# Optimization experiments

Hardware: AMD Instinct MI355X
Metric: run time of the kernel (lower is better)

The kernel has to match this reference:

```python
import jax, jax.numpy as jnp
import numpy as np

U, B, S, R = 64, 256, 256, 512
N = 4096
EMA_DECAY = 0.99


def setup_inputs() -> dict:
    key = jax.random.key(0)
    ks = jax.random.split(key, 9)
    q_u = jax.random.uniform(ks[0], (N, U), dtype=jnp.float32)
    q_b = jax.random.uniform(ks[1], (N, B), dtype=jnp.float32)
    q_sigma = jax.random.normal(ks[2], (N, S), dtype=jnp.float32)
    delta_rule_target = jax.random.normal(ks[3], (N, R), dtype=jnp.float32)
    write_mask = jax.random.randint(ks[4], (N,), 0, 2).astype(bool)
    delta_rule_proto = 0.02 * jax.random.normal(ks[5], (U, B, R), dtype=jnp.float32)
    signature_proto = 0.02 * jax.random.normal(ks[6], (U, B, S), dtype=jnp.float32)
    ema_conf = jax.random.uniform(ks[7], (U, B), dtype=jnp.float32)
    usage_count = jnp.maximum(jax.random.uniform(ks[8], (U, B)) - 0.5, 0.0) * 100.0
    return {"q_u": q_u, "q_b": q_b, "q_sigma": q_sigma,
            "delta_rule_target": delta_rule_target, "write_mask": write_mask,
            "delta_rule_proto": delta_rule_proto, "signature_proto": signature_proto,
            "ema_conf": ema_conf, "usage_count": usage_count}


def _l2norm(x):
    return x / jnp.maximum(jnp.linalg.norm(x, axis=-1, keepdims=True), 1e-12)


def reference(q_u, q_b, q_sigma, delta_rule_target, write_mask,
              delta_rule_proto, signature_proto, ema_conf, usage_count):
    # ---------------- retrieve ----------------
    # joint attention over (operator, binding) cells; temperature == 1.0 branch
    joint = q_u[:, :, None] * q_b[:, None, :]                  # [N, U, B]
    valid = (usage_count > 0).astype(joint.dtype)              # [U, B]
    w = joint * valid
    denom = w.sum(axis=(-2, -1), keepdims=True)
    w = jnp.where(denom > 0, w / jnp.maximum(denom, 1e-6), jnp.zeros_like(w))
    memory_delta_rule = jnp.einsum('nub,ubr->nr', w, delta_rule_proto)
    memory_signature = jnp.einsum('nub,ubs->ns', w, signature_proto)
    base_conf = jnp.einsum('nub,ub->n', w, ema_conf)[:, None]  # [N, 1]
    cos = jnp.sum(_l2norm(q_sigma) * _l2norm(memory_signature + 1e-6),
                  axis=-1, keepdims=True)
    signature_agreement = 0.5 * (1.0 + cos)
    memory_conf = jnp.clip(base_conf * signature_agreement, 0.0, 1.0)

    # ---------------- update (vectorized scatter EMA) ----------------
    m = write_mask.astype(q_u.dtype)                           # [N]
    op_conf = q_u.max(axis=-1)
    op_id = jnp.argmax(q_u, axis=-1)
    bind_conf = q_b.max(axis=-1)
    bind_id = jnp.argmax(q_b, axis=-1)
    write_conf = op_conf * bind_conf                           # [N]
    cell = op_id * B + bind_id                                 # [N]
    num_cells = U * B
    wgt = write_conf * m
    sum_w = jax.ops.segment_sum(wgt, cell, num_segments=num_cells)          # [UB]
    sum_d = jax.ops.segment_sum(delta_rule_target * wgt[:, None], cell,
                                num_segments=num_cells)                     # [UB, R]
    sum_s = jax.ops.segment_sum(q_sigma * wgt[:, None], cell,
                                num_segments=num_cells)                     # [UB, S]
    cnt = jax.ops.segment_sum(m, cell, num_segments=num_cells)              # [UB]
    conf_sum = jnp.maximum(sum_w, 1e-6)
    delta_mean = (sum_d / conf_sum[:, None]).reshape(U, B, R)
    sigma_mean = (sum_s / conf_sum[:, None]).reshape(U, B, S)
    conf_mean = (sum_w / jnp.maximum(cnt, 1.0)).reshape(U, B)
    upd = (cnt > 0).reshape(U, B)
    new_delta_proto = jnp.where(upd[:, :, None],
                                EMA_DECAY * delta_rule_proto + (1.0 - EMA_DECAY) * delta_mean,
                                delta_rule_proto)
    new_signature_proto = jnp.where(upd[:, :, None],
                                    EMA_DECAY * signature_proto + (1.0 - EMA_DECAY) * sigma_mean,
                                    signature_proto)
    new_ema_conf = jnp.where(upd,
                             EMA_DECAY * ema_conf + (1.0 - EMA_DECAY) * conf_mean,
                             ema_conf)
    new_usage = usage_count + cnt.reshape(U, B)

    # ---------------- usage stats ----------------
    write_rate = m.mean()
    usage_fraction = (new_usage > 0).astype(jnp.float32).mean()
    dist = new_usage.reshape(-1)
    dist = dist / jnp.maximum(dist.sum(), 1e-6)
    usage_entropy = -(dist * jnp.log(dist + 1e-6)).sum() / np.log(max(2, num_cells))

    return (memory_delta_rule, memory_signature, memory_conf,
            new_delta_proto, new_signature_proto, new_ema_conf, new_usage,
            write_rate, usage_fraction, usage_entropy)
```

## Files before the change

### kernel.cpp

```cpp
#include <hip/hip_runtime.h>
#include <hip/hip_fp8.h>
#include <math.h>

#define NR 4096
#define UD 64
#define BD 256
#define SD 256
#define RD 512
#define UBD 16384
#define DECAY 0.99f

typedef unsigned char u8;
typedef __attribute__((ext_vector_type(4))) float f32x4;
typedef __attribute__((ext_vector_type(2))) long longx2;

#define OFF_MDR   0ull
#define OFF_MSIG  2097152ull
#define OFF_MCONF 3145728ull
#define OFF_NDP   3149824ull
#define OFF_NSP   11538432ull
#define OFF_NEC   15732736ull
#define OFF_NUS   15749120ull
#define OFF_SCAL  15765504ull

static __device__ __forceinline__ u8 f2e4m3(float x) {
  __hip_fp8_e4m3 h(x);
  return (u8)h.__x;
}

static __device__ __forceinline__ void gll16(const void* g, void* l) {
  __builtin_amdgcn_global_load_lds(
      (const __attribute__((address_space(1))) unsigned int*)g,
      (__attribute__((address_space(3))) unsigned int*)l, 16, 0, 0);
}

static __device__ __forceinline__ int perm64(int x) {
  return (((x >> 3) & 3) << 4) | (((x >> 5) & 1) << 3) | (x & 7);
}

__global__ __launch_bounds__(256) void row_prep_kernel(
    const float* __restrict__ q_u, const float* __restrict__ q_b,
    const float* __restrict__ usage, const float* __restrict__ ema,
    const unsigned char* __restrict__ wm,
    float* __restrict__ denom, float* __restrict__ base_raw,
    float* __restrict__ wgt, int* __restrict__ cellid, float* __restrict__ mrow,
    float* __restrict__ sum_w, float* __restrict__ cnt)
{
  const int r0 = blockIdx.x * 16;
  const int t = threadIdx.x;
  __shared__ float s_qu[16][64];
  __shared__ float s_qbv[16][256];
  __shared__ float s_pd[16][256];
  __shared__ float s_pc[16][256];
  __shared__ int s_flag;
  {
    const float4 v = *(const float4*)(q_u + (size_t)r0 * UD + t * 4);
    float* dst = &s_qu[0][0] + t * 4;
    dst[0] = v.x; dst[1] = v.y; dst[2] = v.z; dst[3] = v.w;
  }
  {
    const float4* src = (const float4*)(q_b + (size_t)r0 * BD);
    float4* dst = (float4*)&s_qbv[0][0];
    #pragma unroll
    for (int i = 0; i < 4; ++i) dst[t + i * 256] = src[t + i * 256];
  }
  if (t == 0) {
    const int*   wi = (const int*)wm;
    const float* wf = (const float*)wm;
    bool is_i32 = true, is_f32 = true;
    #pragma unroll
    for (int i = 0; i < 16; ++i) {
      int v = wi[i];
      if (v != 0 && v != 1) is_i32 = false;
      float f = wf[i];
      if (f != 0.f && f != 1.f) is_f32 = false;
    }
    s_flag = is_i32 ? 2 : (is_f32 ? 1 : 0);
  }
  __syncthreads();
  float accd[16], accc[16];
  #pragma unroll
  for (int r = 0; r < 16; ++r) { accd[r] = 0.f; accc[r] = 0.f; }
  #pragma unroll 2
  for (int u = 0; u < UD; ++u) {
    const float us = usage[u * BD + t];
    const float em = ema[u * BD + t];
    const float vm = (us > 0.f) ? 1.f : 0.f;
    const float ev = em * vm;
    #pragma unroll
    for (int r = 0; r < 16; ++r) {
      accd[r] += s_qu[r][u] * vm;
      accc[r] += s_qu[r][u] * ev;
    }
  }
  #pragma unroll
  for (int r = 0; r < 16; ++r) {
    s_pd[r][t] = accd[r] * s_qbv[r][t];
    s_pc[r][t] = accc[r] * s_qbv[r][t];
  }
  __syncthreads();
  const int w = t >> 6, l = t & 63;
  #pragma unroll
  for (int rr = 0; rr < 4; ++rr) {
    const int row = w * 4 + rr;
    float dsum = s_pd[row][l] + s_pd[row][l + 64] + s_pd[row][l + 128] + s_pd[row][l + 192];
    float csum = s_pc[row][l] + s_pc[row][l + 64] + s_pc[row][l + 128] + s_pc[row][l + 192];
    #pragma unroll
    for (int m = 1; m < 64; m <<= 1) {
      dsum += __shfl_xor(dsum, m);
      csum += __shfl_xor(csum, m);
    }
    float bv_ = s_qbv[row][l]; int bi_ = l;
    #pragma unroll
    for (int k = 1; k < 4; ++k) {
      const float v2 = s_qbv[row][l + k * 64];
      if (v2 > bv_) { bv_ = v2; bi_ = l + k * 64; }
    }
    #pragma unroll
    for (int m = 1; m < 64; m <<= 1) {
      const float ov = __shfl_xor(bv_, m);
      const int   oi = __shfl_xor(bi_, m);
      if (ov > bv_ || (ov == bv_ && oi < bi_)) { bv_ = ov; bi_ = oi; }
    }
    float uv_ = s_qu[row][l]; int ui_ = l;
    #pragma unroll
    for (int m = 1; m < 64; m <<= 1) {
      const float ov = __shfl_xor(uv_, m);
      const int   oi = __shfl_xor(ui_, m);
      if (ov > uv_ || (ov == uv_ && oi < ui_)) { uv_ = ov; ui_ = oi; }
    }
    if (l == 0) {
      const int n = r0 + row;
      const int fm = s_flag;
      float m;
      if (fm == 2)      m = (((const int*)wm)[n]   != 0)   ? 1.f : 0.f;
      else if (fm == 1) m = (((const float*)wm)[n] != 0.f) ? 1.f : 0.f;
      else              m = (wm[n] != 0)   ? 1.f : 0.f;
      const float wv = uv_ * bv_ * m;
      const int cell = ui_ * BD + bi_;
      denom[n]    = dsum;
      base_raw[n] = csum;
      wgt[n]      = wv;
      cellid[n]   = cell;
      mrow[n]     = m;
      if (m != 0.f) {
        atomicAdd(&sum_w[cell], wv);
        atomicAdd(&cnt[cell], 1.f);
      }
    }
  }
}

__global__ __launch_bounds__(256) void prep_kernel(
    const float* __restrict__ qb, const float* __restrict__ qu,
    u8* __restrict__ qb8, float* __restrict__ quT)
{
  if (blockIdx.x < 1024) {
    const int i = blockIdx.x * 256 + threadIdx.x;
    const int idx = i * 4;
    const int row = idx >> 8;
    const int b   = idx & 255;
    const float4 v = *(const float4*)(qb + (size_t)idx);
    u8 tmp[4] = { f2e4m3(v.x), f2e4m3(v.y), f2e4m3(v.z), f2e4m3(v.w) };
    unsigned int wv; __builtin_memcpy(&wv, tmp, 4);
    const int nb = (b & ~63) | perm64(b & 63);
    *(unsigned int*)(qb8 + (size_t)row * BD + nb) = wv;
  } else {
    __shared__ float s[64][65];
    const int n0 = (blockIdx.x - 1024) * 64;
    const int tid = threadIdx.x;
    #pragma unroll
    for (int i = 0; i < 16; ++i) {
      const int idx = tid + i * 256;
      const int r = idx >> 6, u = idx & 63;
      s[r][u] = qu[(size_t)(n0 + r) * UD + u];
    }
    __syncthreads();
    #pragma unroll
    for (int i = 0; i < 16; ++i) {
      const int idx = tid + i * 256;
      const int u = idx >> 6, r = idx & 63;
      quT[(size_t)u * NR + n0 + r] = s[r][u];
    }
  }
}

__global__ __launch_bounds__(256) void transpose_mask_kernel(
    const float* __restrict__ dproto, const float* __restrict__ sproto,
    const float* __restrict__ usage, u8* __restrict__ PT8)
{
  __shared__ u8 s[64][68];
  const int k0 = blockIdx.x * 64;
  const int rblk = blockIdx.y;
  const float* src; int ld; int c0s;
  if (rblk < 8) { src = dproto; ld = RD; c0s = rblk * 64; }
  else          { src = sproto; ld = SD; c0s = (rblk - 8) * 64; }
  const int tid = threadIdx.x;
  const int kl = tid >> 4;
  const int rl = (tid & 15) * 4;
  #pragma unroll
  for (int i = 0; i < 4; ++i) {
    const int k = kl + i * 16;
    const bool valid = usage[k0 + k] > 0.f;
    const float4 v = *(const float4*)(src + (size_t)(k0 + k) * ld + c0s + rl);
    s[k][rl + 0] = valid ? f2e4m3(v.x) : (u8)0;
    s[k][rl + 1] = valid ? f2e4m3(v.y) : (u8)0;
    s[k][rl + 2] = valid ? f2e4m3(v.z) : (u8)0;
    s[k][rl + 3] = valid ? f2e4m3(v.w) : (u8)0;
  }
  __syncthreads();
  const int rl2 = tid >> 4;
  const int kl2 = (tid & 15) * 4;
  #pragma unroll
  for (int i = 0; i < 4; ++i) {
    const int r = rl2 + i * 16;
    u8 tmp[4] = { s[kl2 + 0][r], s[kl2 + 1][r], s[kl2 + 2][r], s[kl2 + 3][r] };
    unsigned int wv; __builtin_memcpy(&wv, tmp, 4);
    *(unsigned int*)(PT8 + (size_t)(rblk * 64 + r) * UBD + k0 + perm64(kl2)) = wv;
  }
}

__global__ __launch_bounds__(256, 3) void mfma_gemm_kernel(
    const float* __restrict__ quT, const u8* __restrict__ qb8,
    const u8* __restrict__ PT8, float* __restrict__ out,
    int* __restrict__ tk, int* __restrict__ gf, int* __restrict__ claimed)
{
  __shared__ u8 sA[2][128 * 128];
  __shared__ u8 sB[2][128 * 64];
  __shared__ int s_work;
  const int tid = threadIdx.x;

  if (tid == 0) {
    unsigned int xcc;
    asm volatile("s_getreg_b32 %0, hwreg(HW_REG_XCC_ID)" : "=s"(xcc));
    const int x = (int)(xcc & 7u);
    const int t = atomicAdd(&tk[x], 1);
    int w = -1;
    if (t < 96) {
      const int cand = x * 96 + t;
      if (atomicCAS(&claimed[cand], 0, 1) == 0) w = cand;
    }
    while (w < 0) {
      const int g = atomicAdd(gf, 1);
      if (g >= 768) { w = -2; break; }
      if (atomicCAS(&claimed[g], 0, 1) == 0) w = g;
    }
    s_work = w;
  }
  __syncthreads();
  const int w = s_work;
  if (w < 0) return;

  const int bx = w & 31;
  const int combo = w >> 5;
  const int by = combo >> 2;
  const int bz = combo & 3;

  const int wid = tid >> 6, lane = tid & 63;
  const int n0 = bx * 128;
  const int kbeg = bz * (UBD / 4);

  float* obase; int ldO; int cc0;
  if (by < 4) { obase = out + OFF_MDR;  ldO = RD; cc0 = by * 128; }
  else        { obase = out + OFF_MSIG; ldO = SD; cc0 = (by - 4) * 128; }
  const int c0 = by * 128;

  const int lrowA = lane >> 3;
  const int csrcA = ((lane & 7) ^ lrowA) * 16;
  const u8* gA = qb8 + (size_t)(n0 + lrowA) * BD + csrcA;
  const int lrowB = lane >> 2;
  const int srcslotB = (lane & 3) ^ ((lrowB >> 1) & 3);
  const u8* gB = PT8 + (size_t)(c0 + wid * 16 + lrowB) * UBD + kbeg + srcslotB * 16;

  const int wr = (wid >> 1) * 64, wc = (wid & 1) * 64;
  const int fr = lane & 15;
  const int kg = lane >> 4;
  int aoff[4], boff[4];
  #pragma unroll
  for (int m = 0; m < 4; ++m) aoff[m] = (wr + m * 16 + fr) * 128;
  #pragma unroll
  for (int nn = 0; nn < 4; ++nn) boff[nn] = (wc + nn * 16 + fr) * 64;
  int slothA[2];
  #pragma unroll
  for (int bq = 0; bq < 2; ++bq) slothA[bq] = ((bq * 4 + kg) ^ (fr & 7)) * 16;
  const int slotB16 = (kg ^ ((fr >> 1) & 3)) * 16;

  f32x4 accm[4][4];
  #pragma unroll
  for (int m = 0; m < 4; ++m)
    #pragma unroll
    for (int nn = 0; nn < 4; ++nn)
      accm[m][nn] = (f32x4){0.f, 0.f, 0.f, 0.f};

  #pragma unroll
  for (int i = 0; i < 4; ++i) {
    const int ro = wid * 32 + i * 8;
    gll16(gA + (size_t)ro * BD,       &sA[0][ro * 128]);
    gll16(gA + (size_t)ro * BD + 128, &sA[1][ro * 128]);
  }
  #pragma unroll
  for (int i = 0; i < 2; ++i)
    gll16(gB + (size_t)(i * 64) * UBD, &sB[0][(i * 64 + wid * 16) * 64]);
  __syncthreads();

  const float* quTb = quT + n0 + wr + kg * 4;
  const int ubase = kbeg >> 8;
  f32x4 accu[4][4];

  for (int ph = 0; ph < 64; ++ph) {
    const int buf  = ph & 1;
    const int half = (ph >> 1) & 1;
    const int bq   = ph & 1;
    if (ph < 63) {
      const u8* gs = gB + (size_t)(ph + 1) * 64;
      #pragma unroll
      for (int i = 0; i < 2; ++i)
        gll16(gs + (size_t)(i * 64) * UBD, &sB[buf ^ 1][(i * 64 + wid * 16) * 64]);
    }
    const u8* sa = sA[half];
    const u8* sb = sB[buf];
    longx2 av[4], bv[4];
    #pragma unroll
    for (int m = 0; m < 4; ++m)
      av[m] = *(const longx2*)(sa + aoff[m] + slothA[bq]);
    #pragma unroll
    for (int nn = 0; nn < 4; ++nn)
      bv[nn] = *(const longx2*)(sb + boff[nn] + slotB16);
    const bool first = (ph & 3) == 0;
    #pragma unroll
    for (int m = 0; m < 4; ++m)
      #pragma unroll
      for (int nn = 0; nn < 4; ++nn) {
        if (first)
          accu[m][nn] = __builtin_amdgcn_mfma_f32_16x16x32_fp8_fp8(
              av[m].x, bv[nn].x, (f32x4){0.f, 0.f, 0.f, 0.f}, 0, 0, 0);
        else
          accu[m][nn] = __builtin_amdgcn_mfma_f32_16x16x32_fp8_fp8(
              av[m].x, bv[nn].x, accu[m][nn], 0, 0, 0);
        accu[m][nn] = __builtin_amdgcn_mfma_f32_16x16x32_fp8_fp8(
            av[m].y, bv[nn].y, accu[m][nn], 0, 0, 0);
      }
    __syncthreads();
    if ((ph & 3) == 3) {
      const float* qp = quTb + (size_t)(ubase + (ph >> 2)) * NR;
      #pragma unroll
      for (int m = 0; m < 4; ++m) {
        const f32x4 qv = *(const f32x4*)(qp + m * 16);
        #pragma unroll
        for (int nn = 0; nn < 4; ++nn)
          accm[m][nn] += qv * accu[m][nn];
      }
    }
  }

  #pragma unroll
  for (int m = 0; m < 4; ++m) {
    #pragma unroll
    for (int nn = 0; nn < 4; ++nn) {
      const int c = cc0 + wc + nn * 16 + fr;
      #pragma unroll
      for (int j = 0; j < 4; ++j) {
        const int r = n0 + wr + m * 16 + kg * 4 + j;
        atomicAdd(obase + (size_t)r * ldO + c, accm[m][nn][j]);
      }
    }
  }
}

__global__ __launch_bounds__(256) void epilogue_kernel(
    const float* __restrict__ q_sigma, const float* __restrict__ denom,
    const float* __restrict__ base_raw, float* __restrict__ out)
{
  const int n = blockIdx.x;
  const int t = threadIdx.x;
  __shared__ float r1[256], r2[256], r3[256];
  const float d = denom[n];
  const float scale = (d > 0.f) ? (1.f / fmaxf(d, 1e-6f)) : 0.f;
  float* mdr = out + OFF_MDR + (size_t)n * RD;
  mdr[t]       *= scale;
  mdr[t + 256] *= scale;
  float* msig = out + OFF_MSIG + (size_t)n * SD;
  const float s = msig[t] * scale;
  msig[t] = s;
  const float a = q_sigma[(size_t)n * SD + t];
  const float b = s + 1e-6f;
  r1[t] = a * a; r2[t] = b * b; r3[t] = a * b;
  __syncthreads();
  for (int st = 128; st > 0; st >>= 1) {
    if (t < st) { r1[t] += r1[t + st]; r2[t] += r2[t + st]; r3[t] += r3[t + st]; }
    __syncthreads();
  }
  if (t == 0) {
    const float na = fmaxf(sqrtf(r1[0]), 1e-12f);
    const float nb = fmaxf(sqrtf(r2[0]), 1e-12f);
    const float cosv = r3[0] / (na * nb);
    const float agree = 0.5f * (1.f + cosv);
    const float base = (d > 0.f) ? base_raw[n] / fmaxf(d, 1e-6f) : 0.f;
    out[OFF_MCONF + n] = fminf(fmaxf(base * agree, 0.f), 1.f);
  }
}

__global__ __launch_bounds__(256) void ema_copy_kernel(
    const float* __restrict__ dproto, const float* __restrict__ sproto,
    const float* __restrict__ cnt,
    float* __restrict__ outd, float* __restrict__ outs)
{
  const size_t nd = (size_t)UBD * RD;
  const size_t total = nd + (size_t)UBD * SD;
  for (size_t i = (size_t)blockIdx.x * 256 + threadIdx.x; i < total;
       i += (size_t)gridDim.x * 256) {
    if (i < nd) {
      const float p = dproto[i];
      outd[i] = (cnt[(int)(i >> 9)] > 0.f) ? DECAY * p : p;
    } else {
      const size_t j = i - nd;
      const float p = sproto[j];
      outs[j] = (cnt[(int)(j >> 8)] > 0.f) ? DECAY * p : p;
    }
  }
}

__global__ __launch_bounds__(256) void scatter2_kernel(
    const float* __restrict__ dtarget, const float* __restrict__ q_sigma,
    const float* __restrict__ wgt, const int* __restrict__ cellid,
    const float* __restrict__ mrow, const float* __restrict__ sum_w,
    float* __restrict__ outd, float* __restrict__ outs)
{
  const int n = blockIdx.x;
  if (mrow[n] == 0.f) return;
  const int t = threadIdx.x;
  const int c = cellid[n];
  const float cs = fmaxf(sum_w[c], 1e-6f);
  const float coef = (1.0f - DECAY) * wgt[n] / cs;
  atomicAdd(&outd[(size_t)c * RD + t],       dtarget[(size_t)n * RD + t] * coef);
  atomicAdd(&outd[(size_t)c * RD + t + 256], dtarget[(size_t)n * RD + t + 256] * coef);
  atomicAdd(&outs[(size_t)c * SD + t],       q_sigma[(size_t)n * SD + t] * coef);
}

__global__ __launch_bounds__(256) void ema_small_kernel(
    const float* __restrict__ ema, const float* __restrict__ usage,
    const float* __restrict__ sum_w, const float* __restrict__ cnt,
    float* __restrict__ out_ec, float* __restrict__ out_us)
{
  const int i = blockIdx.x * 256 + threadIdx.x;
  if (i < UBD) {
    const float c = cnt[i];
    const float cm = sum_w[i] / fmaxf(c, 1.f);
    out_ec[i] = (c > 0.f) ? DECAY * ema[i] + (1.f - DECAY) * cm : ema[i];
    out_us[i] = usage[i] + c;
  }
}

__global__ __launch_bounds__(256) void stats_kernel(
    const float* __restrict__ cnt, const float* __restrict__ new_us,
    float* __restrict__ out_scalars)
{
  const int t = threadIdx.x;
  __shared__ float r1[256], r2[256], r3[256];
  float scnt = 0.f, snz = 0.f, sus = 0.f;
  for (int i = t; i < UBD; i += 256) {
    const float c = cnt[i]; scnt += c;
    const float u = new_us[i];
    if (u > 0.f) snz += 1.f;
    sus += u;
  }
  r1[t] = scnt; r2[t] = snz; r3[t] = sus;
  __syncthreads();
  for (int s = 128; s > 0; s >>= 1) {
    if (t < s) { r1[t] += r1[t + s]; r2[t] += r2[t + s]; r3[t] += r3[t + s]; }
    __syncthreads();
  }
  const float total_cnt = r1[0], total_nz = r2[0], total_us = r3[0];
  __syncthreads();
  const float S = fmaxf(total_us, 1e-6f);
  float ent = 0.f;
  for (int i = t; i < UBD; i += 256) {
    const float d = new_us[i] / S;
    ent += d * logf(d + 1e-6f);
  }
  r1[t] = ent;
  __syncthreads();
  for (int s = 128; s > 0; s >>= 1) {
    if (t < s) { r1[t] += r1[t + s]; }
    __syncthreads();
  }
  if (t == 0) {
    out_scalars[0] = total_cnt / (float)NR;
    out_scalars[1] = total_nz / (float)UBD;
    out_scalars[2] = -r1[0] / 9.70406053f;
  }
}

extern "C" void kernel_launch(void* const* d_in, const int* in_sizes, int n_in,
                              void* d_out, int out_size, void* d_ws, size_t ws_size,
                              hipStream_t stream)
{
  const float* q_u    = (const float*)d_in[0];
  const float* q_b    = (const float*)d_in[1];
  const float* q_sig  = (const float*)d_in[2];
  const float* dtg    = (const float*)d_in[3];
  const unsigned char* wm = (const unsigned char*)d_in[4];
  const float* dproto = (const float*)d_in[5];
  const float* sproto = (const float*)d_in[6];
  const float* ema    = (const float*)d_in[7];
  const float* usage  = (const float*)d_in[8];
  float* out = (float*)d_out;

  float* wsf = (float*)d_ws;
  int*   wsi = (int*)d_ws;
  float* denom    = wsf + 16;
  float* base_raw = wsf + 16 + 4096;
  float* wgtb     = wsf + 16 + 8192;
  int*   cellid   = wsi + 16 + 12288;
  float* mrow     = wsf + 16 + 16384;
  float* sum_w    = wsf + 20496;
  float* cnt      = wsf + 20496 + 16384;
  int*   tk       = wsi + 53264;
  int*   gf       = wsi + 53272;
  int*   claimed  = wsi + 53280;

  u8*    PT8 = (u8*)(out + OFF_NDP);
  u8*    qb8 = PT8 + (size_t)768 * UBD;
  float* quT = (float*)(qb8 + (size_t)NR * BD);

  prep_kernel<<<1024 + NR / 64, 256, 0, stream>>>(q_b, q_u, qb8, quT);
  transpose_mask_kernel<<<dim3(UBD / 64, 12), 256, 0, stream>>>(dproto, sproto,
                                                                usage, PT8);
  hipMemsetAsync(out, 0, (size_t)OFF_MCONF * sizeof(float), stream);
  hipMemsetAsync(sum_w, 0, (2u * UBD + 16 + 768) * sizeof(float), stream);

  row_prep_kernel<<<NR / 16, 256, 0, stream>>>(q_u, q_b, usage, ema, wm,
                                               denom, base_raw, wgtb, cellid, mrow,
                                               sum_w, cnt);
  mfma_gemm_kernel<<<768, 256, 0, stream>>>(quT, qb8, PT8, out, tk, gf, claimed);
  epilogue_kernel<<<NR, 256, 0, stream>>>(q_sig, denom, base_raw, out);

  ema_copy_kernel<<<4096, 256, 0, stream>>>(dproto, sproto, cnt,
                                            out + OFF_NDP, out + OFF_NSP);
  scatter2_kernel<<<NR, 256, 0, stream>>>(dtg, q_sig, wgtb, cellid, mrow, sum_w,
                                          out + OFF_NDP, out + OFF_NSP);
  ema_small_kernel<<<UBD / 256, 256, 0, stream>>>(ema, usage, sum_w, cnt,
                                                  out + OFF_NEC, out + OFF_NUS);
  stats_kernel<<<1, 256, 0, stream>>>(cnt, out + OFF_NUS, out + OFF_SCAL);
}
```

Baseline: 221.7 us.

## Remove split-K from FP8 retrieval GEMM and keep A fragments in registers

The retrieval GEMM drops its 4-way split-K with atomicAdd outputs. It now uses 256 workgroups, each covering 128 rows by 96 columns over the full K range. The q_b FP8 fragments stay in registers, q_u is staged once in LDS, and the prototype tiles stream through a 6-stage LDS ring driven by explicit vmcnt waits. The denominator scaling moves into the GEMM store, which removes the output memset and the read-modify-write in the epilogue. The cost is fewer workgroups (one per CU at launch_bounds 1), longer serial K loops and higher register pressure.

After: 352.6 us. 59.1% more time.

```diff
diff --git a/kernel.cpp b/kernel.cpp
--- a/kernel.cpp
+++ b/kernel.cpp
@@ -220,15 +220,17 @@
   }
 }
 
-__global__ __launch_bounds__(256, 3) void mfma_gemm_kernel(
+__global__ __launch_bounds__(256, 1) void mfma_gemm_kernel(
     const float* __restrict__ quT, const u8* __restrict__ qb8,
-    const u8* __restrict__ PT8, float* __restrict__ out,
+    const u8* __restrict__ PT8, const float* __restrict__ denom,
+    float* __restrict__ out,
     int* __restrict__ tk, int* __restrict__ gf, int* __restrict__ claimed)
 {
-  __shared__ u8 sA[2][128 * 128];
-  __shared__ u8 sB[2][128 * 64];
+  __shared__ __attribute__((aligned(16))) u8 smB[6 * 96 * 128];
+  __shared__ __attribute__((aligned(16))) float squT[64 * 128];
   __shared__ int s_work;
   const int tid = threadIdx.x;
+  const int wid = tid >> 6, lane = tid & 63;
 
   if (tid == 0) {
     unsigned int xcc;
@@ -236,13 +238,13 @@
     const int x = (int)(xcc & 7u);
     const int t = atomicAdd(&tk[x], 1);
     int w = -1;
-    if (t < 96) {
-      const int cand = x * 96 + t;
+    if (t < 32) {
+      const int cand = x * 32 + t;
       if (atomicCAS(&claimed[cand], 0, 1) == 0) w = cand;
     }
     while (w < 0) {
       const int g = atomicAdd(gf, 1);
-      if (g >= 768) { w = -2; break; }
+      if (g >= 256) { w = -2; break; }
       if (atomicCAS(&claimed[g], 0, 1) == 0) w = g;
     }
     s_work = w;
@@ -251,139 +253,135 @@
   const int w = s_work;
   if (w < 0) return;
 
+  const int ct = w >> 5;
   const int bx = w & 31;
-  const int combo = w >> 5;
-  const int by = combo >> 2;
-  const int bz = combo & 3;
-
-  const int wid = tid >> 6, lane = tid & 63;
   const int n0 = bx * 128;
-  const int kbeg = bz * (UBD / 4);
-
-  float* obase; int ldO; int cc0;
-  if (by < 4) { obase = out + OFF_MDR;  ldO = RD; cc0 = by * 128; }
-  else        { obase = out + OFF_MSIG; ldO = SD; cc0 = (by - 4) * 128; }
-  const int c0 = by * 128;
-
-  const int lrowA = lane >> 3;
-  const int csrcA = ((lane & 7) ^ lrowA) * 16;
-  const u8* gA = qb8 + (size_t)(n0 + lrowA) * BD + csrcA;
-  const int lrowB = lane >> 2;
-  const int srcslotB = (lane & 3) ^ ((lrowB >> 1) & 3);
-  const u8* gB = PT8 + (size_t)(c0 + wid * 16 + lrowB) * UBD + kbeg + srcslotB * 16;
-
-  const int wr = (wid >> 1) * 64, wc = (wid & 1) * 64;
+  const int c0 = ct * 96;
+
   const int fr = lane & 15;
   const int kg = lane >> 4;
-  int aoff[4], boff[4];
-  #pragma unroll
-  for (int m = 0; m < 4; ++m) aoff[m] = (wr + m * 16 + fr) * 128;
-  #pragma unroll
-  for (int nn = 0; nn < 4; ++nn) boff[nn] = (wc + nn * 16 + fr) * 64;
-  int slothA[2];
-  #pragma unroll
-  for (int bq = 0; bq < 2; ++bq) slothA[bq] = ((bq * 4 + kg) ^ (fr & 7)) * 16;
-  const int slotB16 = (kg ^ ((fr >> 1) & 3)) * 16;
-
-  f32x4 accm[4][4];
-  #pragma unroll
-  for (int m = 0; m < 4; ++m)
-    #pragma unroll
-    for (int nn = 0; nn < 4; ++nn)
-      accm[m][nn] = (f32x4){0.f, 0.f, 0.f, 0.f};
-
-  #pragma unroll
-  for (int i = 0; i < 4; ++i) {
-    const int ro = wid * 32 + i * 8;
-    gll16(gA + (size_t)ro * BD,       &sA[0][ro * 128]);
-    gll16(gA + (size_t)ro * BD + 128, &sA[1][ro * 128]);
-  }
-  #pragma unroll
-  for (int i = 0; i < 2; ++i)
-    gll16(gB + (size_t)(i * 64) * UBD, &sB[0][(i * 64 + wid * 16) * 64]);
-  __syncthreads();
-
-  const float* quTb = quT + n0 + wr + kg * 4;
-  const int ubase = kbeg >> 8;
-  f32x4 accu[4][4];
-
-  for (int ph = 0; ph < 64; ++ph) {
-    const int buf  = ph & 1;
-    const int half = (ph >> 1) & 1;
-    const int bq   = ph & 1;
-    if (ph < 63) {
-      const u8* gs = gB + (size_t)(ph + 1) * 64;
-      #pragma unroll
-      for (int i = 0; i < 2; ++i)
-        gll16(gs + (size_t)(i * 64) * UBD, &sB[buf ^ 1][(i * 64 + wid * 16) * 64]);
-    }
-    const u8* sa = sA[half];
-    const u8* sb = sB[buf];
-    longx2 av[4], bv[4];
-    #pragma unroll
-    for (int m = 0; m < 4; ++m)
-      av[m] = *(const longx2*)(sa + aoff[m] + slothA[bq]);
-    #pragma unroll
-    for (int nn = 0; nn < 4; ++nn)
-      bv[nn] = *(const longx2*)(sb + boff[nn] + slotB16);
-    const bool first = (ph & 3) == 0;
+  const int wr = (wid >> 1) * 64;
+  const int wcol = (wid & 1) * 48;
+
+  const int lrow = lane >> 3;
+  const int ssl  = ((lane & 7) ^ lrow) * 16;
+  const u8* gB = PT8 + (size_t)(c0 + wid * 24 + lrow) * UBD + ssl;
+
+  int boff[3];
+  #pragma unroll
+  for (int nn = 0; nn < 3; ++nn)
+    boff[nn] = (wcol + nn * 16 + fr) * 128 + ((kg ^ (fr & 7)) << 4);
+
+  longx2 afrag[4][4];
+  {
+    const u8* ga = qb8 + (size_t)(n0 + wr + fr) * BD + kg * 16;
     #pragma unroll
     for (int m = 0; m < 4; ++m)
       #pragma unroll
-      for (int nn = 0; nn < 4; ++nn) {
-        if (first)
+      for (int q = 0; q < 4; ++q)
+        afrag[m][q] = *(const longx2*)(ga + (size_t)m * 16 * BD + q * 64);
+  }
+
+  #pragma unroll
+  for (int i2 = 0; i2 < 8; ++i2) {
+    const int i = wid * 8 + i2;
+    const float* src = quT + (size_t)(i * 2 + (lane >> 5)) * NR + n0 + (lane & 31) * 4;
+    gll16(src, (u8*)squT + i * 1024);
+  }
+  #pragma unroll
+  for (int c = 0; c < 5; ++c)
+    #pragma unroll
+    for (int j = 0; j < 3; ++j)
+      gll16(gB + (size_t)(j * 8) * UBD + c * 128,
+            smB + c * 12288 + (wid * 24 + j * 8) * 128);
+
+  f32x4 accm[4][3], accu[4][3];
+  #pragma unroll
+  for (int m = 0; m < 4; ++m)
+    #pragma unroll
+    for (int nn = 0; nn < 3; ++nn)
+      accm[m][nn] = (f32x4){0.f, 0.f, 0.f, 0.f};
+
+  for (int ph = 0; ph < 128; ++ph) {
+    const int rem = 127 - ph;
+    if (rem >= 4)      asm volatile("s_waitcnt vmcnt(12)" ::: "memory");
+    else if (rem == 3) asm volatile("s_waitcnt vmcnt(9)"  ::: "memory");
+    else if (rem == 2) asm volatile("s_waitcnt vmcnt(6)"  ::: "memory");
+    else if (rem == 1) asm volatile("s_waitcnt vmcnt(3)"  ::: "memory");
+    else               asm volatile("s_waitcnt vmcnt(0)"  ::: "memory");
+    __builtin_amdgcn_s_barrier();
+    if (ph <= 122) {
+      const int tsl = (ph + 5) % 6;
+      #pragma unroll
+      for (int j = 0; j < 3; ++j)
+        gll16(gB + (size_t)(j * 8) * UBD + (size_t)(ph + 5) * 128,
+              smB + tsl * 12288 + (wid * 24 + j * 8) * 128);
+    }
+    const u8* sb = smB + (ph % 6) * 12288;
+    longx2 bv[3][2];
+    #pragma unroll
+    for (int nn = 0; nn < 3; ++nn) {
+      bv[nn][0] = *(const longx2*)(sb + boff[nn]);
+      bv[nn][1] = *(const longx2*)(sb + (boff[nn] ^ 64));
+    }
+    const bool uf = (ph & 1) == 0;
+    #pragma unroll
+    for (int h = 0; h < 2; ++h) {
+      const int q = (ph & 1) * 2 + h;
+      #pragma unroll
+      for (int m = 0; m < 4; ++m)
+        #pragma unroll
+        for (int nn = 0; nn < 3; ++nn) {
+          if (uf && h == 0)
+            accu[m][nn] = __builtin_amdgcn_mfma_f32_16x16x32_fp8_fp8(
+                afrag[m][q].x, bv[nn][h].x, (f32x4){0.f, 0.f, 0.f, 0.f}, 0, 0, 0);
+          else
+            accu[m][nn] = __builtin_amdgcn_mfma_f32_16x16x32_fp8_fp8(
+                afrag[m][q].x, bv[nn][h].x, accu[m][nn], 0, 0, 0);
           accu[m][nn] = __builtin_amdgcn_mfma_f32_16x16x32_fp8_fp8(
-              av[m].x, bv[nn].x, (f32x4){0.f, 0.f, 0.f, 0.f}, 0, 0, 0);
-        else
-          accu[m][nn] = __builtin_amdgcn_mfma_f32_16x16x32_fp8_fp8(
-              av[m].x, bv[nn].x, accu[m][nn], 0, 0, 0);
-        accu[m][nn] = __builtin_amdgcn_mfma_f32_16x16x32_fp8_fp8(
-            av[m].y, bv[nn].y, accu[m][nn], 0, 0, 0);
-      }
-    __syncthreads();
-    if ((ph & 3) == 3) {
-      const float* qp = quTb + (size_t)(ubase + (ph >> 2)) * NR;
+              afrag[m][q].y, bv[nn][h].y, accu[m][nn], 0, 0, 0);
+        }
+    }
+    if (ph & 1) {
+      const float* qs = squT + (ph >> 1) * 128 + wr + kg * 4;
       #pragma unroll
       for (int m = 0; m < 4; ++m) {
-        const f32x4 qv = *(const f32x4*)(qp + m * 16);
+        const f32x4 qv = *(const f32x4*)(qs + m * 16);
         #pragma unroll
-        for (int nn = 0; nn < 4; ++nn)
+        for (int nn = 0; nn < 3; ++nn)
           accm[m][nn] += qv * accu[m][nn];
       }
     }
+    asm volatile("s_waitcnt lgkmcnt(0)" ::: "memory");
   }
 
   #pragma unroll
   for (int m = 0; m < 4; ++m) {
-    #pragma unroll
-    for (int nn = 0; nn < 4; ++nn) {
-      const int c = cc0 + wc + nn * 16 + fr;
+    const int rbase = n0 + wr + m * 16 + kg * 4;
+    #pragma unroll
+    for (int j = 0; j < 4; ++j) {
+      const float d = denom[rbase + j];
+      const float s = (d > 0.f) ? (1.f / fmaxf(d, 1e-6f)) : 0.f;
       #pragma unroll
-      for (int j = 0; j < 4; ++j) {
-        const int r = n0 + wr + m * 16 + kg * 4 + j;
-        atomicAdd(obase + (size_t)r * ldO + c, accm[m][nn][j]);
+      for (int nn = 0; nn < 3; ++nn) {
+        const int cb = c0 + wcol + nn * 16 + fr;
+        const float v = accm[m][nn][j] * s;
+        if (cb < 512) out[(size_t)(rbase + j) * RD + cb] = v;
+        else          out[OFF_MSIG + (size_t)(rbase + j) * SD + (cb - 512)] = v;
       }
     }
   }
 }
 
-__global__ __launch_bounds__(256) void epilogue_kernel(
+__global__ __launch_bounds__(256) void conf_kernel(
     const float* __restrict__ q_sigma, const float* __restrict__ denom,
     const float* __restrict__ base_raw, float* __restrict__ out)
 {
   const int n = blockIdx.x;
   const int t = threadIdx.x;
   __shared__ float r1[256], r2[256], r3[256];
-  const float d = denom[n];
-  const float scale = (d > 0.f) ? (1.f / fmaxf(d, 1e-6f)) : 0.f;
-  float* mdr = out + OFF_MDR + (size_t)n * RD;
-  mdr[t]       *= scale;
-  mdr[t + 256] *= scale;
-  float* msig = out + OFF_MSIG + (size_t)n * SD;
-  const float s = msig[t] * scale;
-  msig[t] = s;
   const float a = q_sigma[(size_t)n * SD + t];
-  const float b = s + 1e-6f;
+  const float b = out[OFF_MSIG + (size_t)n * SD + t] + 1e-6f;
   r1[t] = a * a; r2[t] = b * b; r3[t] = a * b;
   __syncthreads();
   for (int st = 128; st > 0; st >>= 1) {
@@ -395,6 +393,7 @@
     const float nb = fmaxf(sqrtf(r2[0]), 1e-12f);
     const float cosv = r3[0] / (na * nb);
     const float agree = 0.5f * (1.f + cosv);
+    const float d = denom[n];
     const float base = (d > 0.f) ? base_raw[n] / fmaxf(d, 1e-6f) : 0.f;
     out[OFF_MCONF + n] = fminf(fmaxf(base * agree, 0.f), 1.f);
   }
@@ -526,14 +525,14 @@
   prep_kernel<<<1024 + NR / 64, 256, 0, stream>>>(q_b, q_u, qb8, quT);
   transpose_mask_kernel<<<dim3(UBD / 64, 12), 256, 0, stream>>>(dproto, sproto,
                                                                 usage, PT8);
-  hipMemsetAsync(out, 0, (size_t)OFF_MCONF * sizeof(float), stream);
-  hipMemsetAsync(sum_w, 0, (2u * UBD + 16 + 768) * sizeof(float), stream);
+  hipMemsetAsync(sum_w, 0, (2u * UBD + 16 + 256) * sizeof(float), stream);
 
   row_prep_kernel<<<NR / 16, 256, 0, stream>>>(q_u, q_b, usage, ema, wm,
                                                denom, base_raw, wgtb, cellid, mrow,
                                                sum_w, cnt);
-  mfma_gemm_kernel<<<768, 256, 0, stream>>>(quT, qb8, PT8, out, tk, gf, claimed);
-  epilogue_kernel<<<NR, 256, 0, stream>>>(q_sig, denom, base_raw, out);
+  mfma_gemm_kernel<<<256, 256, 0, stream>>>(quT, qb8, PT8, denom, out,
+                                            tk, gf, claimed);
+  conf_kernel<<<NR, 256, 0, stream>>>(q_sig, denom, base_raw, out);
 
   ema_copy_kernel<<<4096, 256, 0, stream>>>(dproto, sproto, cnt,
                                             out + OFF_NDP, out + OFF_NSP);
```
